# Kernel tuning notes

Measured on AMD Instinct MI355X. Metric: run time of the kernel, lower is better.

The kernel has to match this reference:

```python
import jax, jax.numpy as jnp
import numpy as np

# Module hyperparameters (init_kwargs)
K_VAL = 1.0        # Lorentz curvature parameter k (manifold origin time = 1/sqrt(k))
KSIZE = 9
STRIDE = 1
PAD = 4
B, C, L = 32, 16, 16384   # batch, in_channels (incl. time coord), length
OUT_CH = 64
CONCAT_DIM = 1 + (C - 1) * KSIZE  # 136


def setup_inputs() -> dict:
    key = jax.random.key(0)
    k1, k2 = jax.random.split(key, 2)
    # Build valid Lorentz points: channel 0 is the time coordinate,
    # x0 = sqrt(1/k + ||x_space||^2) so that each length position lies on the manifold.
    space = jax.random.normal(k1, (B, C - 1, L), dtype=jnp.float32)
    time = jnp.sqrt(1.0 / K_VAL + jnp.sum(space * space, axis=1, keepdims=True))
    x = jnp.concatenate([time, space], axis=1)  # [B, C, L]
    # Lorentz FC params: weight maps concat_dim -> (out_channels - 1) spatial dims;
    # the output time coordinate is recomputed from the space norm.
    W = jax.random.normal(k2, (OUT_CH - 1, CONCAT_DIM), dtype=jnp.float32) * (1.0 / np.sqrt(CONCAT_DIM))
    b = jnp.zeros((OUT_CH - 1,), dtype=jnp.float32)
    return {"x": x, "W": W, "b": b}


def reference(x, W, b):
    batch, c, length = x.shape
    k, s, p = KSIZE, STRIDE, PAD
    inv_sqrt_k = (1.0 / K_VAL) ** 0.5
    # Pad with the Lorentz origin: time coord = 1/sqrt(k), space coords = 0
    pad_time = jnp.full((batch, 1, p), inv_sqrt_k, dtype=x.dtype)
    pad_space = jnp.zeros((batch, c - 1, p), dtype=x.dtype)
    pad_block = jnp.concatenate([pad_time, pad_space], axis=1)  # [B, C, p]
    xp = jnp.concatenate([pad_block, x, pad_block], axis=2)     # [B, C, L+2p]
    l_pad = length + 2 * p
    num_patches = (l_pad - k) // s + 1
    # im2col unfold: overlapping windows of size k along length
    idx = jnp.arange(num_patches)[:, None] * s + jnp.arange(k)[None, :]  # [P, k]
    patches = xp[:, :, idx]                      # [B, C, P, k]
    patches = jnp.transpose(patches, (0, 2, 3, 1))  # [B, P, k, C]
    # Lorentz direct_concat: concat spatial parts of the k points, recompute time
    space = patches[..., 1:].reshape(batch, num_patches, k * (c - 1))  # [B, P, (C-1)*k]
    time = jnp.sqrt(1.0 / K_VAL + jnp.sum(space * space, axis=-1, keepdims=True))
    concat = jnp.concatenate([time, space], axis=-1)  # [B, P, concat_dim]
    # Lorentz FC ('ours'): space = relu(W x + b); time = sqrt(1/k + ||space||^2)
    h = jax.nn.relu(jnp.einsum('bpd,od->bpo', concat, W) + b)  # [B, P, OUT_CH-1]
    t_out = jnp.sqrt(1.0 / K_VAL + jnp.sum(h * h, axis=-1, keepdims=True))
    out = jnp.concatenate([t_out, h], axis=-1)  # [B, P, OUT_CH]
    return jnp.transpose(out, (0, 2, 1))        # [B, OUT_CH, P]
```

## Files before the change

### kernel.cpp

```cpp
#include <hip/hip_runtime.h>
#include <math.h>

typedef __bf16 bf16x8 __attribute__((ext_vector_type(8)));
typedef float f32x4 __attribute__((ext_vector_type(4)));
typedef unsigned short u16t;

namespace {
constexpr int B_ = 32, CIN = 16, CSP = 15, L_ = 16384;
constexpr int KS = 9, PAD = 4, OUTC = 64, NW = 63, CD = 136;
constexpr int PP = 256;
constexpr int KT = 160;
constexpr int NKS = 5;
constexpr int XR = 268;
constexpr int RSTR = 24;

constexpr int OFF_XT = 0;
constexpr int OFF_CSQ = OFF_XT + XR * RSTR * 2;
constexpr int OFF_RED = ((OFF_CSQ + XR * 4 + 15) / 16) * 16;
constexpr int LDS_BYTES = OFF_RED + 4 * PP * 4;
static_assert(LDS_BYTES <= 60 * 1024, "LDS overflow");

__device__ inline u16t f2bf(float v) {
  unsigned ui = __float_as_uint(v);
  return (u16t)((ui + 0x7fffu + ((ui >> 16) & 1u)) >> 16);
}
__device__ inline float bf2f(u16t u) { return __uint_as_float(((unsigned)u) << 16); }
}

__global__ void prep_w(const float* __restrict__ W, u16t* __restrict__ wbf) {
  int i = blockIdx.x * 256 + threadIdx.x;
  if (i >= OUTC * KT) return;
  int o = i / KT, kk = i - o * KT;
  int jt = kk >> 4, cs = kk & 15;
  float v = 0.f;
  if (o < NW && jt < KS && cs < CSP) v = W[o * CD + 1 + jt * CSP + cs];
  wbf[i] = f2bf(v);
}

__global__ __launch_bounds__(256, 6)
void lorentz_mfma(const float* __restrict__ x, const float* __restrict__ W,
                  const float* __restrict__ bias, const u16t* __restrict__ wbf,
                  float* __restrict__ out) {
  __shared__ __align__(16) char lds[LDS_BYTES];
  const int tid = threadIdx.x;
  const int b = blockIdx.y;
  const int p0 = blockIdx.x * PP;
  const int wv = tid >> 6;
  const int lane = tid & 63;
  const int q = lane >> 4, r = lane & 15;
  const int jtq = q >> 1, half = q & 1;
  const int row = 16 * wv + r;

  u16t* Xt = (u16t*)(lds + OFF_XT);
  float* csq = (float*)(lds + OFF_CSQ);
  float* red = (float*)(lds + OFF_RED);

  uint4 wfrag[NKS];
#pragma unroll
  for (int ks = 0; ks < NKS; ++ks)
    wfrag[ks] = *(const uint4*)(wbf + row * KT + ks * 32 + q * 8);
  const float w0v = (row < NW) ? W[row * CD] : 0.f;
  const float bv = (row < NW) ? bias[row] : 0.f;

  for (int t = tid; t < XR; t += 256) Xt[t * RSTR + 15] = 0;
  for (int e4 = tid; e4 < CSP * (XR / 4); e4 += 256) {
    int cs = e4 / (XR / 4);
    int t4 = e4 - cs * (XR / 4);
    int t = 4 * t4;
    int g0 = p0 - PAD + t;
    const float* src = x + ((size_t)b * CIN + cs + 1) * L_ + g0;
    float v0, v1, v2, v3;
    if (g0 >= 0 && g0 + 3 < L_) {
      float4 v = *(const float4*)src;
      v0 = v.x; v1 = v.y; v2 = v.z; v3 = v.w;
    } else {
      v0 = (g0 >= 0 && g0 < L_) ? src[0] : 0.f;
      v1 = (g0 + 1 >= 0 && g0 + 1 < L_) ? src[1] : 0.f;
      v2 = (g0 + 2 >= 0 && g0 + 2 < L_) ? src[2] : 0.f;
      v3 = (g0 + 3 >= 0 && g0 + 3 < L_) ? src[3] : 0.f;
    }
    u16t* dst = Xt + t * RSTR + cs;
    dst[0] = f2bf(v0);
    dst[RSTR] = f2bf(v1);
    dst[2 * RSTR] = f2bf(v2);
    dst[3 * RSTR] = f2bf(v3);
  }
  __syncthreads();

  for (int t = tid; t < XR; t += 256) {
    const uint4* rw = (const uint4*)(Xt + t * RSTR);
    uint4 a = rw[0], c = rw[1];
    unsigned wds[8] = {a.x, a.y, a.z, a.w, c.x, c.y, c.z, c.w};
    float s = 0.f;
#pragma unroll
    for (int i = 0; i < 8; ++i) {
      float lo = bf2f((u16t)(wds[i] & 0xffffu));
      float hi = bf2f((u16t)(wds[i] >> 16));
      s = fmaf(lo, lo, s);
      s = fmaf(hi, hi, s);
    }
    csq[t] = s;
  }
  __syncthreads();

#pragma unroll 4
  for (int s = 0; s < 16; ++s) {
    bf16x8 av[NKS];
#pragma unroll
    for (int ks = 0; ks < NKS; ++ks) {
      int xrow = s * 16 + r + 2 * ks + jtq;
      av[ks] = *(const bf16x8*)(lds + OFF_XT + xrow * (RSTR * 2) + half * 16);
    }
    f32x4 accA = {0.f, 0.f, 0.f, 0.f}, accB = {0.f, 0.f, 0.f, 0.f};
    {
      union { uint4 u; bf16x8 v; } w0, w1, w2, w3, w4;
      w0.u = wfrag[0]; w1.u = wfrag[1]; w2.u = wfrag[2];
      w3.u = wfrag[3]; w4.u = wfrag[4];
      accA = __builtin_amdgcn_mfma_f32_16x16x32_bf16(av[0], w0.v, accA, 0, 0, 0);
      accB = __builtin_amdgcn_mfma_f32_16x16x32_bf16(av[1], w1.v, accB, 0, 0, 0);
      accA = __builtin_amdgcn_mfma_f32_16x16x32_bf16(av[2], w2.v, accA, 0, 0, 0);
      accB = __builtin_amdgcn_mfma_f32_16x16x32_bf16(av[3], w3.v, accB, 0, 0, 0);
      accA = __builtin_amdgcn_mfma_f32_16x16x32_bf16(av[4], w4.v, accA, 0, 0, 0);
    }
    const f32x4 acc = accA + accB;

    const int base = s * 16 + q * 4;
    const f32x4* c4 = (const f32x4*)(csq + base);
    f32x4 ca = c4[0], cm = c4[1], cc = c4[2];
    float v[12] = {ca[0], ca[1], ca[2], ca[3], cm[0], cm[1], cm[2], cm[3],
                   cc[0], cc[1], cc[2], cc[3]};
    float ws0 = ((v[0] + v[1]) + (v[2] + v[3])) + ((v[4] + v[5]) + (v[6] + v[7])) + v[8];
    float ws1 = ws0 - v[0] + v[9];
    float ws2 = ws1 - v[1] + v[10];
    float ws3 = ws2 - v[2] + v[11];
    const float wsv[4] = {ws0, ws1, ws2, ws3};

    float h[4], psum[4];
#pragma unroll
    for (int g = 0; g < 4; ++g) {
      float tmg = sqrtf(1.f + wsv[g]);
      float hh = fmaf(w0v, tmg, acc[g]) + bv;
      hh = fmaxf(hh, 0.f);
      h[g] = hh;
      psum[g] = hh * hh;
    }
    if (row < NW) {
      *(float4*)(out + ((size_t)b * OUTC + row + 1) * L_ + p0 + s * 16 + q * 4) =
          make_float4(h[0], h[1], h[2], h[3]);
    }
#pragma unroll
    for (int m = 1; m <= 8; m <<= 1) {
#pragma unroll
      for (int g = 0; g < 4; ++g) psum[g] += __shfl_xor(psum[g], m, 64);
    }
    if (r == 0) {
      *(f32x4*)(red + wv * PP + s * 16 + q * 4) =
          (f32x4){psum[0], psum[1], psum[2], psum[3]};
    }
  }
  __syncthreads();

  if (wv == 0) {
    const f32x4* r4 = (const f32x4*)red;
    f32x4 s0 = r4[lane], s1 = r4[64 + lane], s2 = r4[128 + lane], s3 = r4[192 + lane];
    float4 t;
    t.x = sqrtf(1.f + s0[0] + s1[0] + s2[0] + s3[0]);
    t.y = sqrtf(1.f + s0[1] + s1[1] + s2[1] + s3[1]);
    t.z = sqrtf(1.f + s0[2] + s1[2] + s2[2] + s3[2]);
    t.w = sqrtf(1.f + s0[3] + s1[3] + s2[3] + s3[3]);
    *(float4*)(out + (size_t)b * OUTC * L_ + p0 + 4 * lane) = t;
  }
}

extern "C" void kernel_launch(void* const* d_in, const int* in_sizes, int n_in,
                              void* d_out, int out_size, void* d_ws, size_t ws_size,
                              hipStream_t stream) {
  const float* x = (const float*)d_in[0];
  const float* W = (const float*)d_in[1];
  const float* bias = (const float*)d_in[2];
  float* out = (float*)d_out;
  u16t* wbf = (u16t*)d_ws;

  hipLaunchKernelGGL(prep_w, dim3((OUTC * KT + 255) / 256), dim3(256), 0, stream, W, wbf);
  hipLaunchKernelGGL(lorentz_mfma, dim3(L_ / PP, B_), dim3(256), 0, stream,
                     x, W, bias, wbf, out);
}
```

Baseline: 58.24 us.

## Stage output tiles through LDS to issue row-contiguous coalesced global stores

Outputs for each 64-position chunk are now written into a padded LDS tile, together with the per-wave partial norm sums. After a barrier, all waves read the tile back and write whole 64-float row segments to global memory, and compute the time channel for that chunk. Before, each lane stored float4 fragments scattered across 16 rows, and the time channel waited for a single final reduction. The aim is wider, more coalesced stores on this output-write-bound kernel. In exchange it adds eight barriers and more LDS, and lowers the launch-bounds occupancy target from 6 to 5. With a row pitch of 65 floats, the 16-byte LDS vector reads are not 16-byte aligned.

New measurement: 77.11 us. 1.32x slower.

```diff
diff --git a/kernel.cpp b/kernel.cpp
--- a/kernel.cpp
+++ b/kernel.cpp
@@ -13,12 +13,13 @@
 constexpr int NKS = 5;
 constexpr int XR = 268;
 constexpr int RSTR = 24;
+constexpr int HP = 65;
 
 constexpr int OFF_XT = 0;
 constexpr int OFF_CSQ = OFF_XT + XR * RSTR * 2;
-constexpr int OFF_RED = ((OFF_CSQ + XR * 4 + 15) / 16) * 16;
-constexpr int LDS_BYTES = OFF_RED + 4 * PP * 4;
-static_assert(LDS_BYTES <= 60 * 1024, "LDS overflow");
+constexpr int OFF_HB = ((OFF_CSQ + XR * 4 + 15) / 16) * 16;
+constexpr int LDS_BYTES = OFF_HB + 67 * HP * 4;
+static_assert(LDS_BYTES <= 64 * 1024, "LDS overflow");
 
 __device__ inline u16t f2bf(float v) {
   unsigned ui = __float_as_uint(v);
@@ -37,7 +38,7 @@
   wbf[i] = f2bf(v);
 }
 
-__global__ __launch_bounds__(256, 6)
+__global__ __launch_bounds__(256, 5)
 void lorentz_mfma(const float* __restrict__ x, const float* __restrict__ W,
                   const float* __restrict__ bias, const u16t* __restrict__ wbf,
                   float* __restrict__ out) {
@@ -53,7 +54,7 @@
 
   u16t* Xt = (u16t*)(lds + OFF_XT);
   float* csq = (float*)(lds + OFF_CSQ);
-  float* red = (float*)(lds + OFF_RED);
+  float* hb = (float*)(lds + OFF_HB);
 
   uint4 wfrag[NKS];
 #pragma unroll
@@ -103,72 +104,86 @@
   }
   __syncthreads();
 
-#pragma unroll 4
-  for (int s = 0; s < 16; ++s) {
-    bf16x8 av[NKS];
-#pragma unroll
-    for (int ks = 0; ks < NKS; ++ks) {
-      int xrow = s * 16 + r + 2 * ks + jtq;
-      av[ks] = *(const bf16x8*)(lds + OFF_XT + xrow * (RSTR * 2) + half * 16);
-    }
-    f32x4 accA = {0.f, 0.f, 0.f, 0.f}, accB = {0.f, 0.f, 0.f, 0.f};
-    {
-      union { uint4 u; bf16x8 v; } w0, w1, w2, w3, w4;
-      w0.u = wfrag[0]; w1.u = wfrag[1]; w2.u = wfrag[2];
-      w3.u = wfrag[3]; w4.u = wfrag[4];
-      accA = __builtin_amdgcn_mfma_f32_16x16x32_bf16(av[0], w0.v, accA, 0, 0, 0);
-      accB = __builtin_amdgcn_mfma_f32_16x16x32_bf16(av[1], w1.v, accB, 0, 0, 0);
-      accA = __builtin_amdgcn_mfma_f32_16x16x32_bf16(av[2], w2.v, accA, 0, 0, 0);
-      accB = __builtin_amdgcn_mfma_f32_16x16x32_bf16(av[3], w3.v, accB, 0, 0, 0);
-      accA = __builtin_amdgcn_mfma_f32_16x16x32_bf16(av[4], w4.v, accA, 0, 0, 0);
-    }
-    const f32x4 acc = accA + accB;
-
-    const int base = s * 16 + q * 4;
-    const f32x4* c4 = (const f32x4*)(csq + base);
-    f32x4 ca = c4[0], cm = c4[1], cc = c4[2];
-    float v[12] = {ca[0], ca[1], ca[2], ca[3], cm[0], cm[1], cm[2], cm[3],
-                   cc[0], cc[1], cc[2], cc[3]};
-    float ws0 = ((v[0] + v[1]) + (v[2] + v[3])) + ((v[4] + v[5]) + (v[6] + v[7])) + v[8];
-    float ws1 = ws0 - v[0] + v[9];
-    float ws2 = ws1 - v[1] + v[10];
-    float ws3 = ws2 - v[2] + v[11];
-    const float wsv[4] = {ws0, ws1, ws2, ws3};
-
-    float h[4], psum[4];
-#pragma unroll
-    for (int g = 0; g < 4; ++g) {
-      float tmg = sqrtf(1.f + wsv[g]);
-      float hh = fmaf(w0v, tmg, acc[g]) + bv;
-      hh = fmaxf(hh, 0.f);
-      h[g] = hh;
-      psum[g] = hh * hh;
-    }
-    if (row < NW) {
-      *(float4*)(out + ((size_t)b * OUTC + row + 1) * L_ + p0 + s * 16 + q * 4) =
-          make_float4(h[0], h[1], h[2], h[3]);
-    }
-#pragma unroll
-    for (int m = 1; m <= 8; m <<= 1) {
-#pragma unroll
-      for (int g = 0; g < 4; ++g) psum[g] += __shfl_xor(psum[g], m, 64);
-    }
-    if (r == 0) {
-      *(f32x4*)(red + wv * PP + s * 16 + q * 4) =
-          (f32x4){psum[0], psum[1], psum[2], psum[3]};
-    }
-  }
-  __syncthreads();
-
-  if (wv == 0) {
-    const f32x4* r4 = (const f32x4*)red;
-    f32x4 s0 = r4[lane], s1 = r4[64 + lane], s2 = r4[128 + lane], s3 = r4[192 + lane];
-    float4 t;
-    t.x = sqrtf(1.f + s0[0] + s1[0] + s2[0] + s3[0]);
-    t.y = sqrtf(1.f + s0[1] + s1[1] + s2[1] + s3[1]);
-    t.z = sqrtf(1.f + s0[2] + s1[2] + s2[2] + s3[2]);
-    t.w = sqrtf(1.f + s0[3] + s1[3] + s2[3] + s3[3]);
-    *(float4*)(out + (size_t)b * OUTC * L_ + p0 + 4 * lane) = t;
+  for (int ch = 0; ch < 4; ++ch) {
+#pragma unroll
+    for (int sl = 0; sl < 4; ++sl) {
+      const int s = ch * 4 + sl;
+      bf16x8 av[NKS];
+#pragma unroll
+      for (int ks = 0; ks < NKS; ++ks) {
+        int xrow = s * 16 + r + 2 * ks + jtq;
+        av[ks] = *(const bf16x8*)(lds + OFF_XT + xrow * (RSTR * 2) + half * 16);
+      }
+      f32x4 accA = {0.f, 0.f, 0.f, 0.f}, accB = {0.f, 0.f, 0.f, 0.f};
+      {
+        union { uint4 u; bf16x8 v; } w0, w1, w2, w3, w4;
+        w0.u = wfrag[0]; w1.u = wfrag[1]; w2.u = wfrag[2];
+        w3.u = wfrag[3]; w4.u = wfrag[4];
+        accA = __builtin_amdgcn_mfma_f32_16x16x32_bf16(av[0], w0.v, accA, 0, 0, 0);
+        accB = __builtin_amdgcn_mfma_f32_16x16x32_bf16(av[1], w1.v, accB, 0, 0, 0);
+        accA = __builtin_amdgcn_mfma_f32_16x16x32_bf16(av[2], w2.v, accA, 0, 0, 0);
+        accB = __builtin_amdgcn_mfma_f32_16x16x32_bf16(av[3], w3.v, accB, 0, 0, 0);
+        accA = __builtin_amdgcn_mfma_f32_16x16x32_bf16(av[4], w4.v, accA, 0, 0, 0);
+      }
+      const f32x4 acc = accA + accB;
+
+      const int base = s * 16 + q * 4;
+      const f32x4* c4 = (const f32x4*)(csq + base);
+      f32x4 ca = c4[0], cm = c4[1], cc = c4[2];
+      float v[12] = {ca[0], ca[1], ca[2], ca[3], cm[0], cm[1], cm[2], cm[3],
+                     cc[0], cc[1], cc[2], cc[3]};
+      float ws0 = ((v[0] + v[1]) + (v[2] + v[3])) + ((v[4] + v[5]) + (v[6] + v[7])) + v[8];
+      float ws1 = ws0 - v[0] + v[9];
+      float ws2 = ws1 - v[1] + v[10];
+      float ws3 = ws2 - v[2] + v[11];
+      const float wsv[4] = {ws0, ws1, ws2, ws3};
+
+      const int lpos = sl * 16 + q * 4;
+      float psum[4];
+#pragma unroll
+      for (int g = 0; g < 4; ++g) {
+        float tmg = sqrtf(1.f + wsv[g]);
+        float hh = fmaf(w0v, tmg, acc[g]) + bv;
+        hh = fmaxf(hh, 0.f);
+        psum[g] = hh * hh;
+        if (row < NW) hb[(row + 1) * HP + lpos + g] = hh;
+      }
+#pragma unroll
+      for (int m = 1; m <= 8; m <<= 1) {
+#pragma unroll
+        for (int g = 0; g < 4; ++g) psum[g] += __shfl_xor(psum[g], m, 64);
+      }
+      if (r == 0) {
+        const int prow = (wv == 0) ? 0 : (63 + wv);
+#pragma unroll
+        for (int g = 0; g < 4; ++g) hb[prow * HP + lpos + g] = psum[g];
+      }
+    }
+    __syncthreads();
+
+    const int cl = lane >> 4;
+    const int pi = (lane & 15) * 4;
+#pragma unroll
+    for (int i = 0; i < 4; ++i) {
+      const int oc = 16 * wv + 4 * i + cl;
+      if (oc == 0) {
+        f32x4 s0 = *(const f32x4*)&hb[0 * HP + pi];
+        f32x4 s1 = *(const f32x4*)&hb[64 * HP + pi];
+        f32x4 s2 = *(const f32x4*)&hb[65 * HP + pi];
+        f32x4 s3 = *(const f32x4*)&hb[66 * HP + pi];
+        float4 t;
+        t.x = sqrtf(1.f + s0[0] + s1[0] + s2[0] + s3[0]);
+        t.y = sqrtf(1.f + s0[1] + s1[1] + s2[1] + s3[1]);
+        t.z = sqrtf(1.f + s0[2] + s1[2] + s2[2] + s3[2]);
+        t.w = sqrtf(1.f + s0[3] + s1[3] + s2[3] + s3[3]);
+        *(float4*)(out + (size_t)b * OUTC * L_ + p0 + ch * 64 + pi) = t;
+      } else {
+        f32x4 hv = *(const f32x4*)&hb[oc * HP + pi];
+        *(float4*)(out + ((size_t)b * OUTC + oc) * L_ + p0 + ch * 64 + pi) =
+            make_float4(hv[0], hv[1], hv[2], hv[3]);
+      }
+    }
+    __syncthreads();
   }
 }
 
```

## Transpose MFMA outputs through per-wave LDS tile for coalesced stores and cheaper reduction

Applied to the files above, without the earlier changes.

Each wave now computes four 16-position slices into registers, writes them to a per-wave LDS tile, and reads them back transposed. Each store then writes 64 contiguous positions per output row, replacing the 16-position fragments written per slice before. The time-coordinate sum of squares also drops from four xor-shuffle stages per slice to two per group. The cost is extra LDS traffic and about 17 KB more LDS, with launch bounds lowered from 6 to 4 blocks, which may reduce occupancy.

Result: faster. 48.43 us (-16.8%).

```diff
diff --git a/kernel.cpp b/kernel.cpp
--- a/kernel.cpp
+++ b/kernel.cpp
@@ -13,12 +13,14 @@
 constexpr int NKS = 5;
 constexpr int XR = 268;
 constexpr int RSTR = 24;
+constexpr int HTP = 68;
 
 constexpr int OFF_XT = 0;
 constexpr int OFF_CSQ = OFF_XT + XR * RSTR * 2;
-constexpr int OFF_RED = ((OFF_CSQ + XR * 4 + 15) / 16) * 16;
+constexpr int OFF_HT = ((OFF_CSQ + XR * 4 + 15) / 16) * 16;
+constexpr int OFF_RED = OFF_HT + 4 * 16 * HTP * 4;
 constexpr int LDS_BYTES = OFF_RED + 4 * PP * 4;
-static_assert(LDS_BYTES <= 60 * 1024, "LDS overflow");
+static_assert(LDS_BYTES <= 64 * 1024, "LDS overflow");
 
 __device__ inline u16t f2bf(float v) {
   unsigned ui = __float_as_uint(v);
@@ -37,7 +39,7 @@
   wbf[i] = f2bf(v);
 }
 
-__global__ __launch_bounds__(256, 6)
+__global__ __launch_bounds__(256, 4)
 void lorentz_mfma(const float* __restrict__ x, const float* __restrict__ W,
                   const float* __restrict__ bias, const u16t* __restrict__ wbf,
                   float* __restrict__ out) {
@@ -53,6 +55,7 @@
 
   u16t* Xt = (u16t*)(lds + OFF_XT);
   float* csq = (float*)(lds + OFF_CSQ);
+  float* ht = (float*)(lds + OFF_HT) + wv * 16 * HTP;
   float* red = (float*)(lds + OFF_RED);
 
   uint4 wfrag[NKS];
@@ -88,8 +91,8 @@
   __syncthreads();
 
   for (int t = tid; t < XR; t += 256) {
-    const uint4* rw = (const uint4*)(Xt + t * RSTR);
-    uint4 a = rw[0], c = rw[1];
+    const uint4* rw4 = (const uint4*)(Xt + t * RSTR);
+    uint4 a = rw4[0], c = rw4[1];
     unsigned wds[8] = {a.x, a.y, a.z, a.w, c.x, c.y, c.z, c.w};
     float s = 0.f;
 #pragma unroll
@@ -103,60 +106,74 @@
   }
   __syncthreads();
 
-#pragma unroll 4
-  for (int s = 0; s < 16; ++s) {
-    bf16x8 av[NKS];
-#pragma unroll
-    for (int ks = 0; ks < NKS; ++ks) {
-      int xrow = s * 16 + r + 2 * ks + jtq;
-      av[ks] = *(const bf16x8*)(lds + OFF_XT + xrow * (RSTR * 2) + half * 16);
-    }
-    f32x4 accA = {0.f, 0.f, 0.f, 0.f}, accB = {0.f, 0.f, 0.f, 0.f};
-    {
-      union { uint4 u; bf16x8 v; } w0, w1, w2, w3, w4;
-      w0.u = wfrag[0]; w1.u = wfrag[1]; w2.u = wfrag[2];
-      w3.u = wfrag[3]; w4.u = wfrag[4];
-      accA = __builtin_amdgcn_mfma_f32_16x16x32_bf16(av[0], w0.v, accA, 0, 0, 0);
-      accB = __builtin_amdgcn_mfma_f32_16x16x32_bf16(av[1], w1.v, accB, 0, 0, 0);
-      accA = __builtin_amdgcn_mfma_f32_16x16x32_bf16(av[2], w2.v, accA, 0, 0, 0);
-      accB = __builtin_amdgcn_mfma_f32_16x16x32_bf16(av[3], w3.v, accB, 0, 0, 0);
-      accA = __builtin_amdgcn_mfma_f32_16x16x32_bf16(av[4], w4.v, accA, 0, 0, 0);
-    }
-    const f32x4 acc = accA + accB;
-
-    const int base = s * 16 + q * 4;
-    const f32x4* c4 = (const f32x4*)(csq + base);
-    f32x4 ca = c4[0], cm = c4[1], cc = c4[2];
-    float v[12] = {ca[0], ca[1], ca[2], ca[3], cm[0], cm[1], cm[2], cm[3],
-                   cc[0], cc[1], cc[2], cc[3]};
-    float ws0 = ((v[0] + v[1]) + (v[2] + v[3])) + ((v[4] + v[5]) + (v[6] + v[7])) + v[8];
-    float ws1 = ws0 - v[0] + v[9];
-    float ws2 = ws1 - v[1] + v[10];
-    float ws3 = ws2 - v[2] + v[11];
-    const float wsv[4] = {ws0, ws1, ws2, ws3};
-
-    float h[4], psum[4];
+  const int cl = lane >> 4;
+  const int pj = lane & 15;
+  for (int grp = 0; grp < 4; ++grp) {
+    f32x4 hreg[4];
+#pragma unroll
+    for (int sl = 0; sl < 4; ++sl) {
+      const int s = grp * 4 + sl;
+      bf16x8 av[NKS];
+#pragma unroll
+      for (int ks = 0; ks < NKS; ++ks) {
+        int xrow = s * 16 + r + 2 * ks + jtq;
+        av[ks] = *(const bf16x8*)(lds + OFF_XT + xrow * (RSTR * 2) + half * 16);
+      }
+      f32x4 accA = {0.f, 0.f, 0.f, 0.f}, accB = {0.f, 0.f, 0.f, 0.f};
+      {
+        union { uint4 u; bf16x8 v; } w0, w1, w2, w3, w4;
+        w0.u = wfrag[0]; w1.u = wfrag[1]; w2.u = wfrag[2];
+        w3.u = wfrag[3]; w4.u = wfrag[4];
+        accA = __builtin_amdgcn_mfma_f32_16x16x32_bf16(av[0], w0.v, accA, 0, 0, 0);
+        accB = __builtin_amdgcn_mfma_f32_16x16x32_bf16(av[1], w1.v, accB, 0, 0, 0);
+        accA = __builtin_amdgcn_mfma_f32_16x16x32_bf16(av[2], w2.v, accA, 0, 0, 0);
+        accB = __builtin_amdgcn_mfma_f32_16x16x32_bf16(av[3], w3.v, accB, 0, 0, 0);
+        accA = __builtin_amdgcn_mfma_f32_16x16x32_bf16(av[4], w4.v, accA, 0, 0, 0);
+      }
+      const f32x4 acc = accA + accB;
+
+      const int base = s * 16 + q * 4;
+      const f32x4* c4 = (const f32x4*)(csq + base);
+      f32x4 ca = c4[0], cm = c4[1], cc = c4[2];
+      float v[12] = {ca[0], ca[1], ca[2], ca[3], cm[0], cm[1], cm[2], cm[3],
+                     cc[0], cc[1], cc[2], cc[3]};
+      float ws0 = ((v[0] + v[1]) + (v[2] + v[3])) + ((v[4] + v[5]) + (v[6] + v[7])) + v[8];
+      float ws1 = ws0 - v[0] + v[9];
+      float ws2 = ws1 - v[1] + v[10];
+      float ws3 = ws2 - v[2] + v[11];
+      const float wsv[4] = {ws0, ws1, ws2, ws3};
+      f32x4 hh;
+#pragma unroll
+      for (int g = 0; g < 4; ++g) {
+        float tmg = sqrtf(1.f + wsv[g]);
+        hh[g] = fmaxf(fmaf(w0v, tmg, acc[g]) + bv, 0.f);
+      }
+      hreg[sl] = hh;
+    }
+
+#pragma unroll
+    for (int sl = 0; sl < 4; ++sl)
+      *(f32x4*)(ht + r * HTP + sl * 16 + q * 4) = hreg[sl];
+
+    f32x4 ps = {0.f, 0.f, 0.f, 0.f};
+#pragma unroll
+    for (int j = 0; j < 4; ++j) {
+      const int rw = 4 * j + cl;
+      f32x4 hv = *(const f32x4*)(ht + rw * HTP + pj * 4);
+      ps += hv * hv;
+      const int oc = 16 * wv + rw;
+      if (oc < NW) {
+        *(float4*)(out + ((size_t)b * OUTC + oc + 1) * L_ + p0 + grp * 64 + pj * 4) =
+            make_float4(hv[0], hv[1], hv[2], hv[3]);
+      }
+    }
 #pragma unroll
     for (int g = 0; g < 4; ++g) {
-      float tmg = sqrtf(1.f + wsv[g]);
-      float hh = fmaf(w0v, tmg, acc[g]) + bv;
-      hh = fmaxf(hh, 0.f);
-      h[g] = hh;
-      psum[g] = hh * hh;
-    }
-    if (row < NW) {
-      *(float4*)(out + ((size_t)b * OUTC + row + 1) * L_ + p0 + s * 16 + q * 4) =
-          make_float4(h[0], h[1], h[2], h[3]);
-    }
-#pragma unroll
-    for (int m = 1; m <= 8; m <<= 1) {
-#pragma unroll
-      for (int g = 0; g < 4; ++g) psum[g] += __shfl_xor(psum[g], m, 64);
-    }
-    if (r == 0) {
-      *(f32x4*)(red + wv * PP + s * 16 + q * 4) =
-          (f32x4){psum[0], psum[1], psum[2], psum[3]};
-    }
+      ps[g] += __shfl_xor(ps[g], 16, 64);
+      ps[g] += __shfl_xor(ps[g], 32, 64);
+    }
+    if (lane < 16)
+      *(f32x4*)(red + wv * PP + grp * 64 + lane * 4) = ps;
   }
   __syncthreads();
 
```
